# Performance work log

Hardware: AMD Instinct MI355X
Metric: run time of the kernel (lower is better)

The kernel has to match this reference:

```python
import jax, jax.numpy as jnp
import numpy as np

EMBED_DIM = 1024
NUM_HEADS = 16
HEAD_DIM = EMBED_DIM // NUM_HEADS
KERNEL = 3
PAD = KERNEL // 2
B, L = 4, 1024


def conv1d(x, w, b):
    # x: [B, D, L], w: [D_out, D_in, K], b: [D_out]; 'same' padding like nn.Conv1d(padding=K//2)
    y = jax.lax.conv_general_dilated(
        x, w, window_strides=(1,), padding=[(PAD, PAD)],
        dimension_numbers=('NCH', 'OIH', 'NCH'))
    return y + b[None, :, None]


def setup_inputs() -> dict:
    key = jax.random.key(0)
    ks = jax.random.split(key, 12)
    fan = EMBED_DIM * KERNEL
    bound = 1.0 / np.sqrt(fan)
    def wconv(k):
        return jax.random.uniform(k, (EMBED_DIM, EMBED_DIM, KERNEL), jnp.float32, -bound, bound)
    def bconv(k):
        return jax.random.uniform(k, (EMBED_DIM,), jnp.float32, -bound, bound)
    return {
        'query': jax.random.normal(ks[0], (B, L, EMBED_DIM), jnp.float32),
        'key': jax.random.normal(ks[1], (B, L, EMBED_DIM), jnp.float32),
        'value': jax.random.normal(ks[2], (B, L, EMBED_DIM), jnp.float32),
        'key_padding_mask': jax.random.randint(ks[3], (B, L), 0, 2) > 0,
        'attn_mask': jnp.zeros((L, L), jnp.float32),
        'q_w': wconv(ks[4]), 'q_b': bconv(ks[5]),
        'k_w': wconv(ks[6]), 'k_b': bconv(ks[7]),
        'v_w': wconv(ks[8]), 'v_b': bconv(ks[9]),
        'o_w': wconv(ks[10]), 'o_b': bconv(ks[11]),
    }


def reference(query, key, value, key_padding_mask, attn_mask,
              q_w, q_b, k_w, k_b, v_w, v_b, o_w, o_b):
    scale = HEAD_DIM ** -0.5
    # projections: [B, D, L]
    q = conv1d(jnp.swapaxes(query, 1, 2), q_w, q_b)
    k = conv1d(jnp.swapaxes(key, 1, 2), k_w, k_b)
    v = conv1d(jnp.swapaxes(value, 1, 2), v_w, v_b)
    # [B, H, d, L]
    q = q.reshape(B, NUM_HEADS, HEAD_DIM, L)
    k = k.reshape(B, NUM_HEADS, HEAD_DIM, L)
    v = v.reshape(B, NUM_HEADS, HEAD_DIM, L)
    # scores: [B, H, L, L]
    scores = jnp.einsum('bhdi,bhdj->bhij', q, k) * scale
    scores = scores + attn_mask[None, None, :, :]
    scores = jnp.where(key_padding_mask[:, None, None, :], -jnp.inf, scores)
    attn = jax.nn.softmax(scores, axis=-1)  # dropout p=0 (eval) -> identity
    out = jnp.einsum('bhij,bhdj->bhdi', attn, v)  # [B, H, d, L]
    out = out.reshape(B, EMBED_DIM, L)
    out = conv1d(out, o_w, o_b)
    return jnp.swapaxes(out, 1, 2)  # [B, L, D]
```

## Files before the change

kernel.cpp:

```cpp
#include <hip/hip_runtime.h>
#include <math.h>

#define NB 4
#define NL 1024
#define ND 1024
#define NH 16
#define HD 64
#define XS_ONE 4202496u

typedef __attribute__((ext_vector_type(8))) short bf16x8;
typedef __attribute__((ext_vector_type(4))) float f32x4;

static __device__ __forceinline__ unsigned short f32_to_bf16(float f) {
  unsigned u = __float_as_uint(f);
  u += 0x7FFFu + ((u >> 16) & 1u);
  return (unsigned short)(u >> 16);
}
static __device__ __forceinline__ float bf16_to_f32(unsigned short s) {
  return __uint_as_float(((unsigned)s) << 16);
}
static __device__ __forceinline__ void split1(float x, unsigned short* h, unsigned short* l) {
  unsigned u = __float_as_uint(x);
  *h = (unsigned short)(u >> 16);
  float r = x - __uint_as_float(u & 0xFFFF0000u);
  *l = (unsigned short)(__float_as_uint(r) >> 16);
}
static __device__ __forceinline__ void split8(float4 a, float4 b, bf16x8* hi, bf16x8* lo) {
  unsigned u[8] = {__float_as_uint(a.x), __float_as_uint(a.y),
                   __float_as_uint(a.z), __float_as_uint(a.w),
                   __float_as_uint(b.x), __float_as_uint(b.y),
                   __float_as_uint(b.z), __float_as_uint(b.w)};
  union { unsigned p[4]; bf16x8 v; } H, L;
#pragma unroll
  for (int p = 0; p < 4; ++p) {
    unsigned u0 = u[2 * p], u1 = u[2 * p + 1];
    H.p[p] = __builtin_amdgcn_perm(u1, u0, 0x07060302u);
    unsigned l0 = __float_as_uint(__uint_as_float(u0) - __uint_as_float(u0 & 0xFFFF0000u));
    unsigned l1 = __float_as_uint(__uint_as_float(u1) - __uint_as_float(u1 & 0xFFFF0000u));
    L.p[p] = __builtin_amdgcn_perm(l1, l0, 0x07060302u);
  }
  *hi = H.v; *lo = L.v;
}

__global__ __launch_bounds__(256) void wcvt_kernel(
    const float* __restrict__ w0, const float* __restrict__ w1,
    const float* __restrict__ w2, const float* __restrict__ w3,
    unsigned short* __restrict__ wb, int* __restrict__ flag)
{
  if (blockIdx.x == 0 && blockIdx.y == 0 && threadIdx.x == 0) flag[0] = 0;
  const int t = blockIdx.y;
  const int o = blockIdx.x;
  const float* w = (t == 0) ? w0 : (t == 1) ? w1 : (t == 2) ? w2 : w3;
  unsigned short* hi = wb + (size_t)t * 6 * (1u << 20);
  unsigned short* lo = hi + 3 * (1u << 20);
  const int tid = threadIdx.x;
  float v[12];
  const float* src = w + (size_t)o * (ND * 3) + tid * 12;
#pragma unroll
  for (int j = 0; j < 3; ++j) {
    float4 f = *(const float4*)(src + j * 4);
    v[j * 4 + 0] = f.x; v[j * 4 + 1] = f.y; v[j * 4 + 2] = f.z; v[j * 4 + 3] = f.w;
  }
#pragma unroll
  for (int k = 0; k < 3; ++k) {
    unsigned short hh[4], ll[4];
#pragma unroll
    for (int ii = 0; ii < 4; ++ii) {
      float x = v[ii * 3 + k];
      unsigned short h = f32_to_bf16(x);
      float r = x - bf16_to_f32(h);
      hh[ii] = h; ll[ii] = f32_to_bf16(r);
    }
    size_t dst = (size_t)k * (ND * ND) + (size_t)o * ND + tid * 4;
    *(ushort4*)&hi[dst] = make_ushort4(hh[0], hh[1], hh[2], hh[3]);
    *(ushort4*)&lo[dst] = make_ushort4(ll[0], ll[1], ll[2], ll[3]);
  }
}

__global__ __launch_bounds__(256) void amask_scan(
    const float* __restrict__ a, int* __restrict__ flag)
{
  size_t i = ((size_t)blockIdx.x * 256 + threadIdx.x) * 4;
  float4 v = *(const float4*)&a[i];
  if (v.x != 0.f || v.y != 0.f || v.z != 0.f || v.w != 0.f) atomicOr(flag, 1);
}

__global__ __launch_bounds__(256) void xsplit_kernel(
    const float* __restrict__ x0, const float* __restrict__ x1,
    const float* __restrict__ x2, unsigned short* __restrict__ XS)
{
  const int r = blockIdx.x;
  const int b = blockIdx.y;
  const int t = blockIdx.z;
  unsigned short* hi = XS + (size_t)t * 2 * XS_ONE;
  unsigned short* lo = hi + XS_ONE;
  const size_t o = ((size_t)b * 1026 + r) * ND + threadIdx.x * 4;
  if (r == 0 || r == 1025) {
    ushort4 z = make_ushort4(0, 0, 0, 0);
    *(ushort4*)&hi[o] = z; *(ushort4*)&lo[o] = z;
    return;
  }
  const float* x = (t == 0) ? x0 : (t == 1) ? x1 : x2;
  float4 f = *(const float4*)&x[((size_t)b * NL + (r - 1)) * ND + threadIdx.x * 4];
  unsigned short hs[4], ls[4];
  split1(f.x, &hs[0], &ls[0]); split1(f.y, &hs[1], &ls[1]);
  split1(f.z, &hs[2], &ls[2]); split1(f.w, &hs[3], &ls[3]);
  *(ushort4*)&hi[o] = make_ushort4(hs[0], hs[1], hs[2], hs[3]);
  *(ushort4*)&lo[o] = make_ushort4(ls[0], ls[1], ls[2], ls[3]);
}

template <int MODE, bool PRE>
__global__ __launch_bounds__(256, 3) void conv_mfma3(
    const float* X0, const float* X1, const float* X2,
    const unsigned short* __restrict__ XS,
    const unsigned short* __restrict__ wb,
    const float* b0, const float* b1, const float* b2,
    unsigned short* qh, unsigned short* ql,
    unsigned short* kh, unsigned short* kl, unsigned short* vv,
    float* P)
{
  __shared__ __align__(16) unsigned short AS[8192];
  __shared__ __align__(16) unsigned short Bh[4096];
  __shared__ __align__(16) unsigned short Bl[4096];

  const int tid = threadIdx.x, lane = tid & 63, wave = tid >> 6;
  const int lin = blockIdx.x + 8 * (blockIdx.y + 32 * blockIdx.z);
  const int g = lin & 7, t = lin >> 3;
  const int nb = (g & 3) * 2 + (t & 1);
  const int mb = (g >> 2) * 16 + ((t >> 1) & 15);
  const int z  = t >> 5;
  const int n0 = nb * 128, m0 = mb * 128;
  const int b = m0 >> 10, l0v = m0 & (NL - 1);

  const unsigned short* Wh = (MODE == 0) ? wb + (size_t)z * 6 * (1u << 20) : wb;
  const unsigned short* Wl = Wh + 3 * (1u << 20);
  const unsigned short* Xh = nullptr;
  const unsigned short* Xl = nullptr;
  const float* X = nullptr;
  if (MODE == 1) { Xh = XS; Xl = XS + XS_ONE; }
  else if (PRE)  { Xh = XS + (size_t)z * 2 * XS_ONE; Xl = Xh + XS_ONE; }
  else           { X = (z == 0) ? X0 : (z == 1) ? X1 : X2; }

  const int wm = (wave >> 1) * 64, wn = (wave & 1) * 64;
  const int mrow = lane & 15, quad = lane >> 4;
  const int r16 = lane >> 2, cs = lane & 3;
  const int src_chunk = (cs - (r16 >> 1)) & 3;
  const int bswz = ((quad + (mrow >> 1)) & 3) * 8;

  f32x4 acc[4][4] = {};

  const int kbeg = (MODE == 0) ? 0 : z;
  const int kend = (MODE == 0) ? 3 : z + 1;
  for (int koff = kbeg; koff < kend; ++koff) {
    const bool edge_lo = (!PRE) && (l0v == 0 && koff == 0);
    const bool edge_hi = (!PRE) && (l0v == NL - 128 && koff == 2);
    const int rowbase = b * 1026 + l0v + koff;
    for (int i0 = 0; i0 < ND; i0 += 32) {
#pragma unroll
      for (int s = 0; s < 2; ++s) {
        const int seg = wave * 2 + s;
        const size_t goff = ((size_t)koff << 20) +
                            (size_t)(n0 + seg * 16 + r16) * ND + i0 + src_chunk * 8;
        __builtin_amdgcn_global_load_lds(
            (const __attribute__((address_space(1))) unsigned int*)(Wh + goff),
            (__attribute__((address_space(3))) unsigned int*)&Bh[seg * 512], 16, 0, 0);
        __builtin_amdgcn_global_load_lds(
            (const __attribute__((address_space(1))) unsigned int*)(Wl + goff),
            (__attribute__((address_space(3))) unsigned int*)&Bl[seg * 512], 16, 0, 0);
      }
      if (MODE == 1 || PRE) {
#pragma unroll
        for (int s = 0; s < 2; ++s) {
          const int seg = wave * 2 + s;
          const size_t goff = (size_t)(rowbase + seg * 16 + r16) * ND + i0 + src_chunk * 8;
          __builtin_amdgcn_global_load_lds(
              (const __attribute__((address_space(1))) unsigned int*)(Xh + goff),
              (__attribute__((address_space(3))) unsigned int*)&AS[seg * 512], 16, 0, 0);
          __builtin_amdgcn_global_load_lds(
              (const __attribute__((address_space(1))) unsigned int*)(Xl + goff),
              (__attribute__((address_space(3))) unsigned int*)&AS[4096 + seg * 512], 16, 0, 0);
        }
        __syncthreads();
      } else {
        float* Af = (float*)AS;
#pragma unroll
        for (int j = 0; j < 4; ++j) {
          const int s = (wave * 4 + j) * 64 + lane;
          const int row = s >> 3, sir = s & 7;
          const int chunk = (sir - (row & 7)) & 7;
          int l = l0v + row + koff - 1;
          l = (l < 0) ? 0 : (l > NL - 1 ? NL - 1 : l);
          const float* gp = X + ((size_t)(b << 10) + l) * ND + i0 + chunk * 4;
          __builtin_amdgcn_global_load_lds(
              (const __attribute__((address_space(1))) unsigned int*)gp,
              (__attribute__((address_space(3))) unsigned int*)&Af[(wave * 4 + j) * 256],
              16, 0, 0);
        }
        __syncthreads();
        if (edge_lo || edge_hi) {
          const int er = edge_lo ? 0 : 127;
          if (tid < 8) *(float4*)&Af[er * 32 + tid * 4] = make_float4(0.f, 0.f, 0.f, 0.f);
          __syncthreads();
        }
      }

      bf16x8 ah[4], al[4];
      if (MODE == 1 || PRE) {
#pragma unroll
        for (int mi = 0; mi < 4; ++mi) {
          const int row = wm + mi * 16 + mrow;
          ah[mi] = *(const bf16x8*)&AS[row * 32 + bswz];
          al[mi] = *(const bf16x8*)&AS[4096 + row * 32 + bswz];
        }
      } else {
        const float* Af = (const float*)AS;
#pragma unroll
        for (int mi = 0; mi < 4; ++mi) {
          const int row = wm + mi * 16 + mrow, r7 = row & 7;
          float4 fa = *(const float4*)&Af[row * 32 + (((quad * 2) + r7) & 7) * 4];
          float4 fb = *(const float4*)&Af[row * 32 + (((quad * 2 + 1) + r7) & 7) * 4];
          split8(fa, fb, &ah[mi], &al[mi]);
        }
      }
#pragma unroll
      for (int ni = 0; ni < 4; ++ni) {
        const int brow = wn + ni * 16 + mrow;
        bf16x8 bh = *(const bf16x8*)&Bh[brow * 32 + bswz];
        bf16x8 bl = *(const bf16x8*)&Bl[brow * 32 + bswz];
#pragma unroll
        for (int mi = 0; mi < 4; ++mi) {
          acc[mi][ni] = __builtin_amdgcn_mfma_f32_16x16x32_bf16(ah[mi], bh, acc[mi][ni], 0, 0, 0);
          acc[mi][ni] = __builtin_amdgcn_mfma_f32_16x16x32_bf16(ah[mi], bl, acc[mi][ni], 0, 0, 0);
          acc[mi][ni] = __builtin_amdgcn_mfma_f32_16x16x32_bf16(al[mi], bh, acc[mi][ni], 0, 0, 0);
        }
      }
      __syncthreads();
    }
  }

  if (MODE == 0) {
    const float* bias = (z == 0) ? b0 : (z == 1) ? b1 : b2;
#pragma unroll
    for (int ni = 0; ni < 4; ++ni) {
      const int n = n0 + wn + ni * 16 + mrow;
      const float bv = bias[n];
      const int h2 = n >> 6, dd = n & 63;
#pragma unroll
      for (int mi = 0; mi < 4; ++mi) {
        const int mbase = m0 + wm + mi * 16 + quad * 4;
        f32x4 v = acc[mi][ni];
#pragma unroll
        for (int r = 0; r < 4; ++r) {
          const int l = (mbase + r) & (NL - 1);
          const size_t o = (((size_t)b * NH + h2) * NL + l) * HD + dd;
          float val = v[r] + bv;
          if (z == 0) {
            val *= 0.125f;
            unsigned short hs, ls; split1(val, &hs, &ls);
            qh[o] = hs; ql[o] = ls;
          } else if (z == 1) {
            unsigned short hs, ls; split1(val, &hs, &ls);
            kh[o] = hs; kl[o] = ls;
          } else {
            vv[o] = f32_to_bf16(val);
          }
        }
      }
    }
  } else {
    float* Pz = P + (size_t)z * ((size_t)NB * NL * ND);
#pragma unroll
    for (int ni = 0; ni < 4; ++ni) {
      const int n = n0 + wn + ni * 16 + mrow;
#pragma unroll
      for (int mi = 0; mi < 4; ++mi) {
        const int mbase = m0 + wm + mi * 16 + quad * 4;
        f32x4 v = acc[mi][ni];
#pragma unroll
        for (int r = 0; r < 4; ++r) {
          const int l = (mbase + r) & (NL - 1);
          Pz[((size_t)(b << 10) + l) * ND + n] = v[r];
        }
      }
    }
  }
}

__global__ __launch_bounds__(256) void reduce_kernel(
    const float* __restrict__ P, const float* __restrict__ bias, float* __restrict__ out)
{
  const size_t S = (size_t)NB * NL * ND;
  const size_t idx = ((size_t)blockIdx.x * 256 + threadIdx.x) * 4;
  const int n = (int)(idx & (ND - 1));
  float4 p0 = *(const float4*)&P[idx];
  float4 p1 = *(const float4*)&P[idx + S];
  float4 p2 = *(const float4*)&P[idx + 2 * S];
  float4 bv = *(const float4*)&bias[n];
  float4 r;
  r.x = p0.x + p1.x + p2.x + bv.x;
  r.y = p0.y + p1.y + p2.y + bv.y;
  r.z = p0.z + p1.z + p2.z + bv.z;
  r.w = p0.w + p1.w + p2.w + bv.w;
  *(float4*)&out[idx] = r;
}

__global__ __launch_bounds__(256, 3) void attn_mfma2(
    const unsigned short* __restrict__ qhp, const unsigned short* __restrict__ qlp,
    const unsigned short* __restrict__ khp, const unsigned short* __restrict__ klp,
    const unsigned short* __restrict__ vvp, const int* __restrict__ kpm,
    const float* __restrict__ amask, const int* __restrict__ aflagp,
    unsigned short* __restrict__ AOh, unsigned short* __restrict__ AOl)
{
  __shared__ __align__(16) unsigned short SM[8192 + 4608];
  unsigned short* Kh = SM;
  unsigned short* Kl = SM + 4096;
  unsigned short* Vt = SM + 8192;

  const int tid = threadIdx.x, lane = tid & 63, wave = tid >> 6;
  const int c = lane & 15, quad = lane >> 4;
  const int lin = blockIdx.x;
  const int bh = (lin & 7) + 8 * (lin >> 7);
  const int mt = (lin >> 3) & 15;
  const int b = bh >> 4, h = bh & 15;
  const int m0 = mt * 64;
  const size_t base = (size_t)bh * (NL * HD);
  const int aflag = *aflagp;
  const int mrow = wave * 16 + c;
  const int gm = m0 + mrow;

  if (h == 0 && mt == 0) {
    ushort4 z4 = make_ushort4(0, 0, 0, 0);
    *(ushort4*)&AOh[(size_t)(b * 1026) * ND + tid * 4] = z4;
    *(ushort4*)&AOl[(size_t)(b * 1026) * ND + tid * 4] = z4;
  }
  if (h == 0 && mt == 15) {
    ushort4 z4 = make_ushort4(0, 0, 0, 0);
    *(ushort4*)&AOh[((size_t)(b * 1026) + 1025) * ND + tid * 4] = z4;
    *(ushort4*)&AOl[((size_t)(b * 1026) + 1025) * ND + tid * 4] = z4;
  }

  const int rowo = lane >> 3;
  const int grano = ((lane & 7) - rowo) & 7;

#pragma unroll
  for (int j = 0; j < 2; ++j) {
    const int s = wave * 2 + j;
    const size_t go = base + (size_t)(m0 + s * 8 + rowo) * HD + grano * 8;
    __builtin_amdgcn_global_load_lds(
        (const __attribute__((address_space(1))) unsigned int*)(qhp + go),
        (__attribute__((address_space(3))) unsigned int*)&Kh[s * 512], 16, 0, 0);
    __builtin_amdgcn_global_load_lds(
        (const __attribute__((address_space(1))) unsigned int*)(qlp + go),
        (__attribute__((address_space(3))) unsigned int*)&Kl[s * 512], 16, 0, 0);
  }
  __syncthreads();
  bf16x8 qbh[2], qbl[2];
#pragma unroll
  for (int kb = 0; kb < 2; ++kb) {
    const int cso = ((kb * 4 + quad + mrow) & 7) * 8;
    qbh[kb] = *(const bf16x8*)&Kh[mrow * 64 + cso];
    qbl[kb] = *(const bf16x8*)&Kl[mrow * 64 + cso];
  }

  f32x4 acc[4] = {};
  float m_r = -INFINITY, l_r = 0.0f;
  const int sr = tid >> 2, scq = tid & 3;

  for (int n0t = 0; n0t < NL; n0t += 64) {
    __syncthreads();

    float mval[4][4];
#pragma unroll
    for (int nf = 0; nf < 4; ++nf) {
      int4 pm4 = *(const int4*)&kpm[b * NL + n0t + nf * 16 + quad * 4];
      const int* pmi = &pm4.x;
#pragma unroll
      for (int r = 0; r < 4; ++r) {
        float am = 0.f;
        if (aflag) am = amask[(size_t)gm * NL + (n0t + nf * 16 + quad * 4 + r)];
        mval[nf][r] = pmi[r] ? -INFINITY : am;
      }
    }

#pragma unroll
    for (int j = 0; j < 2; ++j) {
      const int s = wave * 2 + j;
      const size_t go = base + (size_t)(n0t + s * 8 + rowo) * HD + grano * 8;
      __builtin_amdgcn_global_load_lds(
          (const __attribute__((address_space(1))) unsigned int*)(khp + go),
          (__attribute__((address_space(3))) unsigned int*)&Kh[s * 512], 16, 0, 0);
      __builtin_amdgcn_global_load_lds(
          (const __attribute__((address_space(1))) unsigned int*)(klp + go),
          (__attribute__((address_space(3))) unsigned int*)&Kl[s * 512], 16, 0, 0);
    }
#pragma unroll
    for (int ii = 0; ii < 2; ++ii) {
      const int c8 = scq * 2 + ii;
      uint4 u = *(const uint4*)(vvp + base + (size_t)(n0t + sr) * HD + c8 * 8);
      const unsigned short* pe = (const unsigned short*)&u;
#pragma unroll
      for (int e = 0; e < 8; ++e) {
        const int dd = c8 * 8 + e;
        Vt[dd * 72 + (((sr >> 3) + dd) & 7) * 8 + (sr & 7)] = pe[e];
      }
    }
    __syncthreads();

    f32x4 sa[4] = {};
#pragma unroll
    for (int kb = 0; kb < 2; ++kb)
#pragma unroll
      for (int nf = 0; nf < 4; ++nf) {
        const int row = nf * 16 + c;
        const int cso = ((kb * 4 + quad + row) & 7) * 8;
        bf16x8 kah = *(const bf16x8*)&Kh[row * 64 + cso];
        bf16x8 kal = *(const bf16x8*)&Kl[row * 64 + cso];
        sa[nf] = __builtin_amdgcn_mfma_f32_16x16x32_bf16(kah, qbh[kb], sa[nf], 0, 0, 0);
        sa[nf] = __builtin_amdgcn_mfma_f32_16x16x32_bf16(kah, qbl[kb], sa[nf], 0, 0, 0);
        sa[nf] = __builtin_amdgcn_mfma_f32_16x16x32_bf16(kal, qbh[kb], sa[nf], 0, 0, 0);
      }

    float p[4][4];
    float tmax = -INFINITY;
#pragma unroll
    for (int nf = 0; nf < 4; ++nf)
#pragma unroll
      for (int r = 0; r < 4; ++r) {
        float s = sa[nf][r] + mval[nf][r];
        p[nf][r] = s;
        tmax = fmaxf(tmax, s);
      }
    tmax = fmaxf(tmax, __shfl_xor(tmax, 16));
    tmax = fmaxf(tmax, __shfl_xor(tmax, 32));
    const float newm = fmaxf(m_r, tmax);
    const float msafe = (newm == -INFINITY) ? 0.f : newm;
    const float alpha = __expf(m_r - msafe);
    float rs = 0.f;
#pragma unroll
    for (int nf = 0; nf < 4; ++nf)
#pragma unroll
      for (int r = 0; r < 4; ++r) {
        float e = __expf(p[nf][r] - msafe);
        p[nf][r] = e;
        rs += e;
      }
    rs += __shfl_xor(rs, 16);
    rs += __shfl_xor(rs, 32);
    l_r = l_r * alpha + rs;
    m_r = newm;
#pragma unroll
    for (int df = 0; df < 4; ++df) {
      acc[df][0] *= alpha; acc[df][1] *= alpha;
      acc[df][2] *= alpha; acc[df][3] *= alpha;
    }

    unsigned q16[4][2];
#pragma unroll
    for (int nf = 0; nf < 4; ++nf)
#pragma unroll
      for (int w = 0; w < 2; ++w)
        q16[nf][w] = (unsigned)f32_to_bf16(p[nf][2 * w]) |
                     ((unsigned)f32_to_bf16(p[nf][2 * w + 1]) << 16);
#pragma unroll
    for (int kb = 0; kb < 2; ++kb) {
      union { unsigned d[4]; bf16x8 v; } pb;
#pragma unroll
      for (int w = 0; w < 4; ++w) {
        const int addr = ((((quad & 1) * 2 + (w >> 1)) * 16 + c) << 2);
        unsigned v0 = __builtin_amdgcn_ds_bpermute(addr, (int)q16[2 * kb][w & 1]);
        unsigned v1 = __builtin_amdgcn_ds_bpermute(addr, (int)q16[2 * kb + 1][w & 1]);
        pb.d[w] = (quad >> 1) ? v1 : v0;
      }
#pragma unroll
      for (int df = 0; df < 4; ++df) {
        const int row = df * 16 + c;
        const int cso = ((kb * 4 + quad + row) & 7) * 8;
        bf16x8 va = *(const bf16x8*)&Vt[row * 72 + cso];
        acc[df] = __builtin_amdgcn_mfma_f32_16x16x32_bf16(va, pb.v, acc[df], 0, 0, 0);
      }
    }
  }

  __syncthreads();
  const float inv = 1.0f / l_r;
  float* Ob = (float*)SM + wave * (16 * 68);
#pragma unroll
  for (int df = 0; df < 4; ++df)
#pragma unroll
    for (int r = 0; r < 4; ++r)
      Ob[c * 68 + df * 16 + quad * 4 + r] = acc[df][r] * inv;
  __syncthreads();
  const int mr2 = lane >> 2, cq2 = lane & 3;
#pragma unroll
  for (int ii = 0; ii < 4; ++ii) {
    const int chunk = cq2 * 4 + ii;
    float4 v = *(const float4*)&Ob[mr2 * 68 + chunk * 4];
    unsigned short hs[4], ls[4];
    split1(v.x, &hs[0], &ls[0]); split1(v.y, &hs[1], &ls[1]);
    split1(v.z, &hs[2], &ls[2]); split1(v.w, &hs[3], &ls[3]);
    const size_t o = ((size_t)(b * 1026) + (m0 + wave * 16 + mr2) + 1) * ND +
                     h * HD + chunk * 4;
    *(ushort4*)&AOh[o] = make_ushort4(hs[0], hs[1], hs[2], hs[3]);
    *(ushort4*)&AOl[o] = make_ushort4(ls[0], ls[1], ls[2], ls[3]);
  }
}

extern "C" void kernel_launch(void* const* d_in, const int* in_sizes, int n_in,
                              void* d_out, int out_size, void* d_ws, size_t ws_size,
                              hipStream_t stream) {
  (void)in_sizes; (void)n_in; (void)out_size;
  const float* query = (const float*)d_in[0];
  const float* key_  = (const float*)d_in[1];
  const float* value = (const float*)d_in[2];
  const int*   kpm   = (const int*)d_in[3];
  const float* amask = (const float*)d_in[4];
  const float* q_w = (const float*)d_in[5];
  const float* q_b = (const float*)d_in[6];
  const float* k_w = (const float*)d_in[7];
  const float* k_b = (const float*)d_in[8];
  const float* v_w = (const float*)d_in[9];
  const float* v_b = (const float*)d_in[10];
  const float* o_w = (const float*)d_in[11];
  const float* o_b = (const float*)d_in[12];
  float* out = (float*)d_out;

  const size_t WB_BYTES = 50331648;
  unsigned short* Wb = (unsigned short*)d_ws;
  const bool big = ws_size >= 142704640ull;
  unsigned short* XSp = (unsigned short*)((char*)d_ws + WB_BYTES);
  char* qkv_base = big ? ((char*)d_ws + 100761600) : ((char*)d_ws + WB_BYTES);
  unsigned short* qh = (unsigned short*)qkv_base;
  unsigned short* ql = qh + 4194304;
  unsigned short* kh = ql + 4194304;
  unsigned short* kl = kh + 4194304;
  unsigned short* vv = kl + 4194304;
  unsigned short* AOh = (unsigned short*)d_ws;
  unsigned short* AOl = AOh + XS_ONE;
  float* P = (float*)((char*)d_ws + WB_BYTES);
  int* flag = (int*)d_out;

  wcvt_kernel<<<dim3(1024, 4), 256, 0, stream>>>(q_w, k_w, v_w, o_w, Wb, flag);
  amask_scan<<<1024, 256, 0, stream>>>(amask, flag);
  if (big) {
    xsplit_kernel<<<dim3(1026, NB, 3), 256, 0, stream>>>(query, key_, value, XSp);
    conv_mfma3<0, true><<<dim3(8, 32, 3), 256, 0, stream>>>(
        nullptr, nullptr, nullptr, XSp, Wb, q_b, k_b, v_b, qh, ql, kh, kl, vv, nullptr);
  } else {
    conv_mfma3<0, false><<<dim3(8, 32, 3), 256, 0, stream>>>(
        query, key_, value, nullptr, Wb, q_b, k_b, v_b, qh, ql, kh, kl, vv, nullptr);
  }
  attn_mfma2<<<1024, 256, 0, stream>>>(qh, ql, kh, kl, vv, kpm, amask, flag, AOh, AOl);
  conv_mfma3<1, true><<<dim3(8, 32, 3), 256, 0, stream>>>(
      nullptr, nullptr, nullptr, AOh, Wb + (size_t)3 * 6 * (1u << 20),
      nullptr, nullptr, nullptr, nullptr, nullptr, nullptr, nullptr, nullptr, P);
  reduce_kernel<<<4096, 256, 0, stream>>>(P, o_b, out);
}
```

Measured before the change: 521.6 us.

## Double-buffer conv GEMM LDS stages and always use pre-split inputs

Rewrites the conv GEMM kernel so the global-to-LDS loads for the next K-slice are issued into a second LDS buffer while MFMAs run on the current one, with a single barrier per step. It also drops the fp32-input fallback path and always runs the xsplit pre-conversion, assuming the workspace is large enough. LDS use doubles and the occupancy hint drops from 3 to 2 blocks per CU, which trades latency hiding from extra waves for software pipelining.

```diff
diff --git a/kernel.cpp b/kernel.cpp
--- a/kernel.cpp
+++ b/kernel.cpp
@@ -24,22 +24,6 @@
   *h = (unsigned short)(u >> 16);
   float r = x - __uint_as_float(u & 0xFFFF0000u);
   *l = (unsigned short)(__float_as_uint(r) >> 16);
-}
-static __device__ __forceinline__ void split8(float4 a, float4 b, bf16x8* hi, bf16x8* lo) {
-  unsigned u[8] = {__float_as_uint(a.x), __float_as_uint(a.y),
-                   __float_as_uint(a.z), __float_as_uint(a.w),
-                   __float_as_uint(b.x), __float_as_uint(b.y),
-                   __float_as_uint(b.z), __float_as_uint(b.w)};
-  union { unsigned p[4]; bf16x8 v; } H, L;
-#pragma unroll
-  for (int p = 0; p < 4; ++p) {
-    unsigned u0 = u[2 * p], u1 = u[2 * p + 1];
-    H.p[p] = __builtin_amdgcn_perm(u1, u0, 0x07060302u);
-    unsigned l0 = __float_as_uint(__uint_as_float(u0) - __uint_as_float(u0 & 0xFFFF0000u));
-    unsigned l1 = __float_as_uint(__uint_as_float(u1) - __uint_as_float(u1 & 0xFFFF0000u));
-    L.p[p] = __builtin_amdgcn_perm(l1, l0, 0x07060302u);
-  }
-  *hi = H.v; *lo = L.v;
 }
 
 __global__ __launch_bounds__(256) void wcvt_kernel(
@@ -109,9 +93,8 @@
   *(ushort4*)&lo[o] = make_ushort4(ls[0], ls[1], ls[2], ls[3]);
 }
 
-template <int MODE, bool PRE>
-__global__ __launch_bounds__(256, 3) void conv_mfma3(
-    const float* X0, const float* X1, const float* X2,
+template <int MODE>
+__global__ __launch_bounds__(256, 2) void conv_mfma4(
     const unsigned short* __restrict__ XS,
     const unsigned short* __restrict__ wb,
     const float* b0, const float* b1, const float* b2,
@@ -119,9 +102,10 @@
     unsigned short* kh, unsigned short* kl, unsigned short* vv,
     float* P)
 {
-  __shared__ __align__(16) unsigned short AS[8192];
-  __shared__ __align__(16) unsigned short Bh[4096];
-  __shared__ __align__(16) unsigned short Bl[4096];
+  __shared__ __align__(16) unsigned short Ah2[2][4096];
+  __shared__ __align__(16) unsigned short Al2[2][4096];
+  __shared__ __align__(16) unsigned short Bh2[2][4096];
+  __shared__ __align__(16) unsigned short Bl2[2][4096];
 
   const int tid = threadIdx.x, lane = tid & 63, wave = tid >> 6;
   const int lin = blockIdx.x + 8 * (blockIdx.y + 32 * blockIdx.z);
@@ -134,12 +118,8 @@
 
   const unsigned short* Wh = (MODE == 0) ? wb + (size_t)z * 6 * (1u << 20) : wb;
   const unsigned short* Wl = Wh + 3 * (1u << 20);
-  const unsigned short* Xh = nullptr;
-  const unsigned short* Xl = nullptr;
-  const float* X = nullptr;
-  if (MODE == 1) { Xh = XS; Xl = XS + XS_ONE; }
-  else if (PRE)  { Xh = XS + (size_t)z * 2 * XS_ONE; Xl = Xh + XS_ONE; }
-  else           { X = (z == 0) ? X0 : (z == 1) ? X1 : X2; }
+  const unsigned short* Xh = (MODE == 0) ? XS + (size_t)z * 2 * XS_ONE : XS;
+  const unsigned short* Xl = Xh + XS_ONE;
 
   const int wm = (wave >> 1) * 64, wn = (wave & 1) * 64;
   const int mrow = lane & 15, quad = lane >> 4;
@@ -149,93 +129,58 @@
 
   f32x4 acc[4][4] = {};
 
-  const int kbeg = (MODE == 0) ? 0 : z;
-  const int kend = (MODE == 0) ? 3 : z + 1;
-  for (int koff = kbeg; koff < kend; ++koff) {
-    const bool edge_lo = (!PRE) && (l0v == 0 && koff == 0);
-    const bool edge_hi = (!PRE) && (l0v == NL - 128 && koff == 2);
+  const int NS = (MODE == 0) ? 96 : 32;
+
+  auto stage = [&](int s, int buf) {
+    const int koff = (MODE == 0) ? (s >> 5) : z;
+    const int i0 = (s & 31) * 32;
     const int rowbase = b * 1026 + l0v + koff;
-    for (int i0 = 0; i0 < ND; i0 += 32) {
-#pragma unroll
-      for (int s = 0; s < 2; ++s) {
-        const int seg = wave * 2 + s;
-        const size_t goff = ((size_t)koff << 20) +
-                            (size_t)(n0 + seg * 16 + r16) * ND + i0 + src_chunk * 8;
-        __builtin_amdgcn_global_load_lds(
-            (const __attribute__((address_space(1))) unsigned int*)(Wh + goff),
-            (__attribute__((address_space(3))) unsigned int*)&Bh[seg * 512], 16, 0, 0);
-        __builtin_amdgcn_global_load_lds(
-            (const __attribute__((address_space(1))) unsigned int*)(Wl + goff),
-            (__attribute__((address_space(3))) unsigned int*)&Bl[seg * 512], 16, 0, 0);
-      }
-      if (MODE == 1 || PRE) {
-#pragma unroll
-        for (int s = 0; s < 2; ++s) {
-          const int seg = wave * 2 + s;
-          const size_t goff = (size_t)(rowbase + seg * 16 + r16) * ND + i0 + src_chunk * 8;
-          __builtin_amdgcn_global_load_lds(
-              (const __attribute__((address_space(1))) unsigned int*)(Xh + goff),
-              (__attribute__((address_space(3))) unsigned int*)&AS[seg * 512], 16, 0, 0);
-          __builtin_amdgcn_global_load_lds(
-              (const __attribute__((address_space(1))) unsigned int*)(Xl + goff),
-              (__attribute__((address_space(3))) unsigned int*)&AS[4096 + seg * 512], 16, 0, 0);
-        }
-        __syncthreads();
-      } else {
-        float* Af = (float*)AS;
-#pragma unroll
-        for (int j = 0; j < 4; ++j) {
-          const int s = (wave * 4 + j) * 64 + lane;
-          const int row = s >> 3, sir = s & 7;
-          const int chunk = (sir - (row & 7)) & 7;
-          int l = l0v + row + koff - 1;
-          l = (l < 0) ? 0 : (l > NL - 1 ? NL - 1 : l);
-          const float* gp = X + ((size_t)(b << 10) + l) * ND + i0 + chunk * 4;
-          __builtin_amdgcn_global_load_lds(
-              (const __attribute__((address_space(1))) unsigned int*)gp,
-              (__attribute__((address_space(3))) unsigned int*)&Af[(wave * 4 + j) * 256],
-              16, 0, 0);
-        }
-        __syncthreads();
-        if (edge_lo || edge_hi) {
-          const int er = edge_lo ? 0 : 127;
-          if (tid < 8) *(float4*)&Af[er * 32 + tid * 4] = make_float4(0.f, 0.f, 0.f, 0.f);
-          __syncthreads();
-        }
-      }
-
-      bf16x8 ah[4], al[4];
-      if (MODE == 1 || PRE) {
-#pragma unroll
-        for (int mi = 0; mi < 4; ++mi) {
-          const int row = wm + mi * 16 + mrow;
-          ah[mi] = *(const bf16x8*)&AS[row * 32 + bswz];
-          al[mi] = *(const bf16x8*)&AS[4096 + row * 32 + bswz];
-        }
-      } else {
-        const float* Af = (const float*)AS;
-#pragma unroll
-        for (int mi = 0; mi < 4; ++mi) {
-          const int row = wm + mi * 16 + mrow, r7 = row & 7;
-          float4 fa = *(const float4*)&Af[row * 32 + (((quad * 2) + r7) & 7) * 4];
-          float4 fb = *(const float4*)&Af[row * 32 + (((quad * 2 + 1) + r7) & 7) * 4];
-          split8(fa, fb, &ah[mi], &al[mi]);
-        }
-      }
-#pragma unroll
-      for (int ni = 0; ni < 4; ++ni) {
-        const int brow = wn + ni * 16 + mrow;
-        bf16x8 bh = *(const bf16x8*)&Bh[brow * 32 + bswz];
-        bf16x8 bl = *(const bf16x8*)&Bl[brow * 32 + bswz];
-#pragma unroll
-        for (int mi = 0; mi < 4; ++mi) {
-          acc[mi][ni] = __builtin_amdgcn_mfma_f32_16x16x32_bf16(ah[mi], bh, acc[mi][ni], 0, 0, 0);
-          acc[mi][ni] = __builtin_amdgcn_mfma_f32_16x16x32_bf16(ah[mi], bl, acc[mi][ni], 0, 0, 0);
-          acc[mi][ni] = __builtin_amdgcn_mfma_f32_16x16x32_bf16(al[mi], bh, acc[mi][ni], 0, 0, 0);
-        }
-      }
-      __syncthreads();
-    }
+#pragma unroll
+    for (int j = 0; j < 2; ++j) {
+      const int seg = wave * 2 + j;
+      const size_t gw = ((size_t)koff << 20) +
+                        (size_t)(n0 + seg * 16 + r16) * ND + i0 + src_chunk * 8;
+      __builtin_amdgcn_global_load_lds(
+          (const __attribute__((address_space(1))) unsigned int*)(Wh + gw),
+          (__attribute__((address_space(3))) unsigned int*)&Bh2[buf][seg * 512], 16, 0, 0);
+      __builtin_amdgcn_global_load_lds(
+          (const __attribute__((address_space(1))) unsigned int*)(Wl + gw),
+          (__attribute__((address_space(3))) unsigned int*)&Bl2[buf][seg * 512], 16, 0, 0);
+      const size_t ga = (size_t)(rowbase + seg * 16 + r16) * ND + i0 + src_chunk * 8;
+      __builtin_amdgcn_global_load_lds(
+          (const __attribute__((address_space(1))) unsigned int*)(Xh + ga),
+          (__attribute__((address_space(3))) unsigned int*)&Ah2[buf][seg * 512], 16, 0, 0);
+      __builtin_amdgcn_global_load_lds(
+          (const __attribute__((address_space(1))) unsigned int*)(Xl + ga),
+          (__attribute__((address_space(3))) unsigned int*)&Al2[buf][seg * 512], 16, 0, 0);
+    }
+  };
+
+  stage(0, 0);
+  __syncthreads();
+  for (int s = 0; s < NS; ++s) {
+    const int buf = s & 1;
+    if (s + 1 < NS) stage(s + 1, buf ^ 1);
+    bf16x8 ah[4], al[4];
+#pragma unroll
+    for (int mi = 0; mi < 4; ++mi) {
+      const int row = wm + mi * 16 + mrow;
+      ah[mi] = *(const bf16x8*)&Ah2[buf][row * 32 + bswz];
+      al[mi] = *(const bf16x8*)&Al2[buf][row * 32 + bswz];
+    }
+#pragma unroll
+    for (int ni = 0; ni < 4; ++ni) {
+      const int brow = wn + ni * 16 + mrow;
+      bf16x8 bh = *(const bf16x8*)&Bh2[buf][brow * 32 + bswz];
+      bf16x8 bl = *(const bf16x8*)&Bl2[buf][brow * 32 + bswz];
+#pragma unroll
+      for (int mi = 0; mi < 4; ++mi) {
+        acc[mi][ni] = __builtin_amdgcn_mfma_f32_16x16x32_bf16(ah[mi], bh, acc[mi][ni], 0, 0, 0);
+        acc[mi][ni] = __builtin_amdgcn_mfma_f32_16x16x32_bf16(ah[mi], bl, acc[mi][ni], 0, 0, 0);
+        acc[mi][ni] = __builtin_amdgcn_mfma_f32_16x16x32_bf16(al[mi], bh, acc[mi][ni], 0, 0, 0);
+      }
+    }
+    __syncthreads();
   }
 
   if (MODE == 0) {
@@ -508,7 +453,7 @@
 extern "C" void kernel_launch(void* const* d_in, const int* in_sizes, int n_in,
                               void* d_out, int out_size, void* d_ws, size_t ws_size,
                               hipStream_t stream) {
-  (void)in_sizes; (void)n_in; (void)out_size;
+  (void)in_sizes; (void)n_in; (void)out_size; (void)ws_size;
   const float* query = (const float*)d_in[0];
   const float* key_  = (const float*)d_in[1];
   const float* value = (const float*)d_in[2];
@@ -526,9 +471,8 @@
 
   const size_t WB_BYTES = 50331648;
   unsigned short* Wb = (unsigned short*)d_ws;
-  const bool big = ws_size >= 142704640ull;
   unsigned short* XSp = (unsigned short*)((char*)d_ws + WB_BYTES);
-  char* qkv_base = big ? ((char*)d_ws + 100761600) : ((char*)d_ws + WB_BYTES);
+  char* qkv_base = (char*)d_ws + 100761600;
   unsigned short* qh = (unsigned short*)qkv_base;
   unsigned short* ql = qh + 4194304;
   unsigned short* kh = ql + 4194304;
@@ -541,17 +485,12 @@
 
   wcvt_kernel<<<dim3(1024, 4), 256, 0, stream>>>(q_w, k_w, v_w, o_w, Wb, flag);
   amask_scan<<<1024, 256, 0, stream>>>(amask, flag);
-  if (big) {
-    xsplit_kernel<<<dim3(1026, NB, 3), 256, 0, stream>>>(query, key_, value, XSp);
-    conv_mfma3<0, true><<<dim3(8, 32, 3), 256, 0, stream>>>(
-        nullptr, nullptr, nullptr, XSp, Wb, q_b, k_b, v_b, qh, ql, kh, kl, vv, nullptr);
-  } else {
-    conv_mfma3<0, false><<<dim3(8, 32, 3), 256, 0, stream>>>(
-        query, key_, value, nullptr, Wb, q_b, k_b, v_b, qh, ql, kh, kl, vv, nullptr);
-  }
+  xsplit_kernel<<<dim3(1026, NB, 3), 256, 0, stream>>>(query, key_, value, XSp);
+  conv_mfma4<0><<<dim3(8, 32, 3), 256, 0, stream>>>(
+      XSp, Wb, q_b, k_b, v_b, qh, ql, kh, kl, vv, nullptr);
   attn_mfma2<<<1024, 256, 0, stream>>>(qh, ql, kh, kl, vv, kpm, amask, flag, AOh, AOl);
-  conv_mfma3<1, true><<<dim3(8, 32, 3), 256, 0, stream>>>(
-      nullptr, nullptr, nullptr, AOh, Wb + (size_t)3 * 6 * (1u << 20),
-      nullptr, nullptr, nullptr, nullptr, nullptr, nullptr, nullptr, nullptr, P);
+  conv_mfma4<1><<<dim3(8, 32, 3), 256, 0, stream>>>(
+      AOh, Wb + (size_t)3 * 6 * (1u << 20), nullptr, nullptr, nullptr,
+      nullptr, nullptr, nullptr, nullptr, nullptr, P);
   reduce_kernel<<<4096, 256, 0, stream>>>(P, o_b, out);
 }
```

Measured after the change: 641.5 us. 1.23x slower.
